# Kernel optimization log

Hardware: AMD Instinct MI355X
Metric: run time of the kernel (lower is better)

## Reference

```python
import jax, jax.numpy as jnp
import numpy as np


def setup_inputs() -> dict:
    key = jax.random.key(0)
    ks = jax.random.split(key, 8)
    B, N, D = 8, 2048, 128
    s = 1.0 / float(np.sqrt(D))
    node = jax.random.normal(ks[0], (B, N, D), dtype=jnp.float32)
    node_mask = jax.random.randint(ks[1], (B, N), 0, 2, dtype=jnp.int32)
    punctuation_graph = jax.random.randint(ks[2], (B, N, N), 0, 2, dtype=jnp.int32)
    w_nw = jax.random.uniform(ks[3], (1, D), jnp.float32, -s, s)
    b_nw = jax.random.uniform(ks[4], (1,), jnp.float32, -s, s)
    w_self = jax.random.uniform(ks[5], (D, D), jnp.float32, -s, s)
    b_self = jax.random.uniform(ks[6], (D,), jnp.float32, -s, s)
    w_punct = jax.random.uniform(ks[7], (D, D), jnp.float32, -s, s)
    return {"node": node, "node_mask": node_mask, "punctuation_graph": punctuation_graph,
            "w_nw": w_nw, "b_nw": b_nw, "w_self": w_self, "b_self": b_self,
            "w_punct": w_punct, "iteration_steps": 2}


def reference(node, node_mask, punctuation_graph, w_nw, b_nw, w_self, b_self, w_punct, iteration_steps):
    B, N, D = node.shape
    # dd_graph = mask outer product with zeroed diagonal; graph = dd_graph * punctuation_graph
    eye = jnp.eye(N, dtype=punctuation_graph.dtype)
    dd = node_mask[:, None, :] * node_mask[:, :, None] * (1 - eye)[None, :, :]  # [B,N,N]
    graph = dd * punctuation_graph  # [B,N,N] int, binary
    nbr_num = graph.sum(-1)  # [B,N]
    # replace_masked_values(nbr_num, nbr_num>=1, 1): nodes with no neighbors get denom 1
    nbr_f = jnp.where(nbr_num >= 1, nbr_num.astype(node.dtype), jnp.asarray(1.0, node.dtype))
    gmask = graph > 0
    weights = []
    x = node
    for _ in range(iteration_steps):  # small fixed step count
        dw = jax.nn.sigmoid(jnp.einsum('bnd,od->bno', x, w_nw) + b_nw)[..., 0]  # [B,N]
        weights.append(dw)
        self_info = jnp.einsum('bnd,ed->bne', x, w_self) + b_self  # [B,N,D]
        info_p = jnp.einsum('bnd,ed->bne', x, w_punct)  # [B,N,D]
        # node_weight[b,i,j] = dw[b,j] where graph[b,i,j] else 0
        nw = jnp.where(gmask, dw[:, None, :], jnp.asarray(0.0, x.dtype))  # [B,N,N]
        agg = jnp.einsum('bnm,bmd->bnd', nw, info_p) / nbr_f[..., None]
        x = jax.nn.relu(self_info + agg)
    all_weight = jnp.stack(weights, axis=1)  # [B, steps, N]
    return x, all_weight
```

## Files before the change

kernel.cpp:

```cpp
#include <hip/hip_runtime.h>
#include <hip/hip_bf16.h>

#define BB 8
#define NN 2048
#define DD 128

typedef __attribute__((ext_vector_type(8))) __bf16 bf16x8;
typedef __attribute__((ext_vector_type(4))) float f32x4;
typedef __attribute__((ext_vector_type(4))) int   i32x4;

static __device__ __forceinline__ unsigned short f2bf(float f) {
    union { float f; unsigned u; } v; v.f = f;
    unsigned r = (v.u + 0x7FFFu + ((v.u >> 16) & 1u)) >> 16;
    return (unsigned short)r;
}
static __device__ __forceinline__ float bf2f(unsigned short b) {
    union { unsigned u; float f; } v; v.u = ((unsigned)b) << 16;
    return v.f;
}

__global__ __launch_bounds__(256) void kernP2(
    const int* __restrict__ punct, const int* __restrict__ mask,
    const float* __restrict__ w_self, const float* __restrict__ w_punct,
    unsigned* __restrict__ pk, float* __restrict__ scale_g, float* __restrict__ pdm_g,
    unsigned short* __restrict__ wsb, unsigned short* __restrict__ wpb)
{
    const int bid = blockIdx.x;
    const int t = threadIdx.x;

    if (bid >= 2048) {
        const int cb = bid - 2048;
        const float* src = (cb < 8) ? w_self : w_punct;
        unsigned short* dst = (cb < 8) ? wsb : wpb;
        const size_t i0 = (size_t)(cb & 7) * 2048 + (size_t)t * 8;
        f32x4 a = *(const f32x4*)(src + i0);
        f32x4 c = *(const f32x4*)(src + i0 + 4);
        unsigned q0 = f2bf(a.x) | ((unsigned)f2bf(a.y) << 16);
        unsigned q1 = f2bf(a.z) | ((unsigned)f2bf(a.w) << 16);
        unsigned q2 = f2bf(c.x) | ((unsigned)f2bf(c.y) << 16);
        unsigned q3 = f2bf(c.z) | ((unsigned)f2bf(c.w) << 16);
        i32x4 pw = {(int)q0, (int)q1, (int)q2, (int)q3};
        *(i32x4*)(dst + i0) = pw;
        return;
    }

    const int wave = t >> 6, lane = t & 63;
    const int row0 = bid * 8 + wave * 2;
    const int b = row0 >> 11;
    const int* mrow = mask + (size_t)b * NN;

    unsigned mreg = 0;
    #pragma unroll
    for (int g = 0; g < 8; ++g) {
        i32x4 m = *(const i32x4*)(mrow + g * 256 + lane * 4);
        unsigned nib = (m.x & 1) | ((m.y & 1) << 1) | ((m.z & 1) << 2) | ((m.w & 1) << 3);
        mreg |= nib << (4 * g);
    }

    #pragma unroll
    for (int r = 0; r < 2; ++r) {
        const int row = row0 + r;
        const int i = row & (NN - 1);
        const int* prow = punct + (size_t)row * NN;
        unsigned* pkrow = pk + (size_t)row * 64;

        int acc = 0;
        #pragma unroll
        for (int g = 0; g < 8; ++g) {
            i32x4 v = *(const i32x4*)(prow + g * 256 + lane * 4);
            unsigned nib = (v.x & 1) | ((v.y & 1) << 1) | ((v.z & 1) << 2) | ((v.w & 1) << 3);
            nib &= (mreg >> (4 * g)) & 0xFu;
            acc += __popc(nib);
            if (((i >> 8) == g) && (((i >> 2) & 63) == lane))
                acc += (int)((nib >> (i & 3)) & 1u) << 16;
            unsigned p1 = __shfl_xor(nib, 1, 64);
            unsigned lo = (lane & 1) ? p1 : nib, hi = (lane & 1) ? nib : p1;
            unsigned by = lo | (hi << 4);
            unsigned p2 = __shfl_xor(by, 2, 64);
            lo = (lane & 2) ? p2 : by; hi = (lane & 2) ? by : p2;
            unsigned hf = lo | (hi << 8);
            unsigned p4 = __shfl_xor(hf, 4, 64);
            lo = (lane & 4) ? p4 : hf; hi = (lane & 4) ? hf : p4;
            unsigned wd = lo | (hi << 16);
            if ((lane & 7) == 0) pkrow[g * 8 + (lane >> 3)] = wd;
        }
        #pragma unroll
        for (int o = 32; o > 0; o >>= 1) acc += __shfl_xor(acc, o, 64);
        if (lane == 0) {
            const int nall = acc & 0xFFFF;
            const int pdm  = acc >> 16;
            const int mi   = mrow[i];
            const int nbr  = nall - pdm;
            scale_g[row] = mi ? 1.f / (float)(nbr < 1 ? 1 : nbr) : 0.f;
            pdm_g[row]   = (float)pdm;
        }
    }
}

template <bool PRECONV>
static __device__ __forceinline__ void kernB_body(
    int n0, const float* __restrict__ x,
    const float* __restrict__ w_nw,  const float* __restrict__ b_nw,
    const void* __restrict__ wself_p, const float* __restrict__ b_self,
    const void* __restrict__ wpunct_p,
    float* __restrict__ si_out,
    unsigned short* __restrict__ yne_out,
    unsigned short* __restrict__ yT_out,
    float* __restrict__ aw_out)
{
    __shared__ unsigned short xt[64*32];
    __shared__ unsigned short wst[128*32];
    __shared__ unsigned short wpt[128*32];
    __shared__ float wnw_l[DD];
    __shared__ float red[256];
    __shared__ float dw_l[64];
    __shared__ unsigned short ytl[128*72];

    const int t  = threadIdx.x;
    const int b  = n0 >> 11;
    const int nb = n0 & (NN - 1);

    if (t < DD) wnw_l[t] = w_nw[t];
    __syncthreads();

    const int wave = t >> 6, lane = t & 63;
    const int wm = wave >> 1, wn = wave & 1;
    const int quad = lane >> 4, l16 = lane & 15;

    const int n_loc = t >> 2, dq = t & 3;
    const int we = t >> 1,   wh = t & 1;

    f32x4 accs[2][4] = {}; f32x4 accp[2][4] = {};
    float dwpart = 0.f;

    #pragma unroll
    for (int kk = 0; kk < 4; ++kk) {
        const int k0 = kk * 32;
        {
            const float* xs = x + (size_t)(n0 + n_loc) * DD + k0 + dq * 8;
            f32x4 a = *(const f32x4*)xs;
            f32x4 c = *(const f32x4*)(xs + 4);
            const float* wv = &wnw_l[k0 + dq * 8];
            dwpart += a.x*wv[0] + a.y*wv[1] + a.z*wv[2] + a.w*wv[3]
                    + c.x*wv[4] + c.y*wv[5] + c.z*wv[6] + c.w*wv[7];
            unsigned q0 = f2bf(a.x) | ((unsigned)f2bf(a.y) << 16);
            unsigned q1 = f2bf(a.z) | ((unsigned)f2bf(a.w) << 16);
            unsigned q2 = f2bf(c.x) | ((unsigned)f2bf(c.y) << 16);
            unsigned q3 = f2bf(c.z) | ((unsigned)f2bf(c.w) << 16);
            i32x4 pw = {(int)q0,(int)q1,(int)q2,(int)q3};
            *(i32x4*)&xt[n_loc*32 + dq*8] = pw;
        }
        if (PRECONV) {
            const unsigned short* s1 = (const unsigned short*)wself_p  + (size_t)we * DD + k0 + wh*16;
            const unsigned short* s2 = (const unsigned short*)wpunct_p + (size_t)we * DD + k0 + wh*16;
            i32x4 a0 = *(const i32x4*)s1;
            i32x4 a1 = *(const i32x4*)(s1 + 8);
            *(i32x4*)&wst[we*32 + wh*16]     = a0;
            *(i32x4*)&wst[we*32 + wh*16 + 8] = a1;
            i32x4 c0 = *(const i32x4*)s2;
            i32x4 c1 = *(const i32x4*)(s2 + 8);
            *(i32x4*)&wpt[we*32 + wh*16]     = c0;
            *(i32x4*)&wpt[we*32 + wh*16 + 8] = c1;
        } else {
            const float* s1 = (const float*)wself_p  + (size_t)we * DD + k0 + wh*16;
            const float* s2 = (const float*)wpunct_p + (size_t)we * DD + k0 + wh*16;
            f32x4 a0 = *(const f32x4*)s1;      f32x4 a1 = *(const f32x4*)(s1+4);
            f32x4 a2 = *(const f32x4*)(s1+8);  f32x4 a3 = *(const f32x4*)(s1+12);
            unsigned q0 = f2bf(a0.x) | ((unsigned)f2bf(a0.y)<<16);
            unsigned q1 = f2bf(a0.z) | ((unsigned)f2bf(a0.w)<<16);
            unsigned q2 = f2bf(a1.x) | ((unsigned)f2bf(a1.y)<<16);
            unsigned q3 = f2bf(a1.z) | ((unsigned)f2bf(a1.w)<<16);
            unsigned q4 = f2bf(a2.x) | ((unsigned)f2bf(a2.y)<<16);
            unsigned q5 = f2bf(a2.z) | ((unsigned)f2bf(a2.w)<<16);
            unsigned q6 = f2bf(a3.x) | ((unsigned)f2bf(a3.y)<<16);
            unsigned q7 = f2bf(a3.z) | ((unsigned)f2bf(a3.w)<<16);
            i32x4 pw0 = {(int)q0,(int)q1,(int)q2,(int)q3};
            i32x4 pw1 = {(int)q4,(int)q5,(int)q6,(int)q7};
            *(i32x4*)&wst[we*32 + wh*16]     = pw0;
            *(i32x4*)&wst[we*32 + wh*16 + 8] = pw1;
            f32x4 c0 = *(const f32x4*)s2;      f32x4 c1 = *(const f32x4*)(s2+4);
            f32x4 c2 = *(const f32x4*)(s2+8);  f32x4 c3 = *(const f32x4*)(s2+12);
            unsigned r0 = f2bf(c0.x) | ((unsigned)f2bf(c0.y)<<16);
            unsigned r1 = f2bf(c0.z) | ((unsigned)f2bf(c0.w)<<16);
            unsigned r2 = f2bf(c1.x) | ((unsigned)f2bf(c1.y)<<16);
            unsigned r3 = f2bf(c1.z) | ((unsigned)f2bf(c1.w)<<16);
            unsigned r4 = f2bf(c2.x) | ((unsigned)f2bf(c2.y)<<16);
            unsigned r5 = f2bf(c2.z) | ((unsigned)f2bf(c2.w)<<16);
            unsigned r6 = f2bf(c3.x) | ((unsigned)f2bf(c3.y)<<16);
            unsigned r7 = f2bf(c3.z) | ((unsigned)f2bf(c3.w)<<16);
            i32x4 pv0 = {(int)r0,(int)r1,(int)r2,(int)r3};
            i32x4 pv1 = {(int)r4,(int)r5,(int)r6,(int)r7};
            *(i32x4*)&wpt[we*32 + wh*16]     = pv0;
            *(i32x4*)&wpt[we*32 + wh*16 + 8] = pv1;
        }
        __syncthreads();
        bf16x8 af[2], bs[4], bp[4];
        #pragma unroll
        for (int mt = 0; mt < 2; ++mt)
            af[mt] = *(const bf16x8*)&xt[(wm*32 + mt*16 + l16)*32 + quad*8];
        #pragma unroll
        for (int nt = 0; nt < 4; ++nt) {
            const int er = wn*64 + nt*16 + l16;
            bs[nt] = *(const bf16x8*)&wst[er*32 + quad*8];
            bp[nt] = *(const bf16x8*)&wpt[er*32 + quad*8];
        }
        #pragma unroll
        for (int mt = 0; mt < 2; ++mt)
            #pragma unroll
            for (int nt = 0; nt < 4; ++nt) {
                accs[mt][nt] = __builtin_amdgcn_mfma_f32_16x16x32_bf16(af[mt], bs[nt], accs[mt][nt], 0, 0, 0);
                accp[mt][nt] = __builtin_amdgcn_mfma_f32_16x16x32_bf16(af[mt], bp[nt], accp[mt][nt], 0, 0, 0);
            }
        __syncthreads();
    }

    red[t] = dwpart;
    __syncthreads();
    if (t < 64) {
        float s = red[4*t] + red[4*t+1] + red[4*t+2] + red[4*t+3] + b_nw[0];
        float dv = 1.f / (1.f + __expf(-s));
        dw_l[t] = dv;
        aw_out[(size_t)b * 2 * NN + nb + t] = dv;
    }
    __syncthreads();

    #pragma unroll
    for (int mt = 0; mt < 2; ++mt) {
        #pragma unroll
        for (int nt = 0; nt < 4; ++nt) {
            const int e = wn*64 + nt*16 + l16;
            const float bsv = b_self[e];
            #pragma unroll
            for (int r = 0; r < 4; ++r) {
                const int nl = wm*32 + mt*16 + quad*4 + r;
                const size_t idx = (size_t)(n0 + nl) * DD + e;
                si_out[idx] = accs[mt][nt][r] + bsv;
                const float yv = dw_l[nl] * accp[mt][nt][r];
                const unsigned short ub = f2bf(yv);
                yne_out[idx] = ub;
                ytl[e*72 + nl] = ub;
            }
        }
    }
    __syncthreads();
    {
        const int e = t >> 1, half = t & 1;
        const i32x4* src = (const i32x4*)&ytl[e*72 + half*32];
        i32x4 v0 = src[0], v1 = src[1], v2 = src[2], v3 = src[3];
        i32x4* dst = (i32x4*)(yT_out + (size_t)(b*DD + e) * NN + nb + half*32);
        dst[0] = v0; dst[1] = v1; dst[2] = v2; dst[3] = v3;
    }
}

__global__ __launch_bounds__(256) void kernB0(
    const float* __restrict__ node,
    const float* __restrict__ w_nw, const float* __restrict__ b_nw,
    const float* __restrict__ w_self, const float* __restrict__ b_self,
    const float* __restrict__ w_punct,
    float* __restrict__ si, unsigned short* __restrict__ yne,
    unsigned short* __restrict__ yT, float* __restrict__ aw)
{
    kernB_body<false>(blockIdx.x * 64, node, w_nw, b_nw, w_self, b_self, w_punct,
                      si, yne, yT, aw);
}

__global__ __launch_bounds__(256) void kernB1(
    const float* __restrict__ x,
    const unsigned short* __restrict__ wsb, const unsigned short* __restrict__ wpb,
    const float* __restrict__ w_nw, const float* __restrict__ b_nw,
    const float* __restrict__ b_self,
    float* __restrict__ si, unsigned short* __restrict__ yne,
    unsigned short* __restrict__ yT, float* __restrict__ aw1)
{
    kernB_body<true>(blockIdx.x * 64, x, w_nw, b_nw, wsb, b_self, wpb,
                     si, yne, yT, aw1);
}

__global__ __launch_bounds__(256) void kernC(
    const unsigned* __restrict__ pk,
    const float* __restrict__ scale_g, const float* __restrict__ pdm_g,
    const unsigned short* __restrict__ yT,
    const float* __restrict__ si,
    const unsigned short* __restrict__ yne,
    float* __restrict__ x_out)
{
    __shared__ unsigned pPk[64 * 68];
    __shared__ float scale_l[64];
    __shared__ float pdm_l[64];

    const int t  = threadIdx.x;
    const int b  = blockIdx.x & 7;
    const int i0 = (blockIdx.x >> 3) * 64;
    const size_t rg0 = (size_t)b * NN + i0;

    #pragma unroll
    for (int r = 0; r < 4; ++r) {
        const int u   = r * 256 + t;
        const int row = u >> 4;
        const int wq  = (u & 15) * 4;
        i32x4 v = *(const i32x4*)(pk + (rg0 + row) * 64 + wq);
        *(i32x4*)&pPk[row * 68 + wq] = v;
    }
    if (t < 64) {
        scale_l[t] = scale_g[rg0 + t];
        pdm_l[t]   = pdm_g[rg0 + t];
    }
    __syncthreads();

    const int wn = t >> 6, lane = t & 63;
    const int quad = lane >> 4, l16 = lane & 15;
    const unsigned short* yTb = yT + (size_t)b * DD * NN;

    f32x4 acc[4][2] = {};

    #pragma unroll 4
    for (int kk = 0; kk < 64; ++kk) {
        bf16x8 bfr[2];
        #pragma unroll
        for (int nt = 0; nt < 2; ++nt) {
            const int e = wn*32 + nt*16 + l16;
            bfr[nt] = *(const bf16x8*)(yTb + (size_t)e * NN + kk*32 + quad*8);
        }
        bf16x8 af[4];
        #pragma unroll
        for (int mt = 0; mt < 4; ++mt) {
            const unsigned w = pPk[(mt*16 + l16) * 68 + kk];
            const unsigned by = (w >> (quad * 8)) & 0xFFu;
            i32x4 ex;
            ex.x = ((by &   1u) ? 0x3F80 : 0) | ((by &   2u) ? 0x3F800000 : 0);
            ex.y = ((by &   4u) ? 0x3F80 : 0) | ((by &   8u) ? 0x3F800000 : 0);
            ex.z = ((by &  16u) ? 0x3F80 : 0) | ((by &  32u) ? 0x3F800000 : 0);
            ex.w = ((by &  64u) ? 0x3F80 : 0) | ((by & 128u) ? 0x3F800000 : 0);
            union { i32x4 i; bf16x8 h; } cv; cv.i = ex;
            af[mt] = cv.h;
        }
        #pragma unroll
        for (int mt = 0; mt < 4; ++mt)
            #pragma unroll
            for (int nt = 0; nt < 2; ++nt)
                acc[mt][nt] = __builtin_amdgcn_mfma_f32_16x16x32_bf16(af[mt], bfr[nt], acc[mt][nt], 0, 0, 0);
    }

    #pragma unroll
    for (int mt = 0; mt < 4; ++mt) {
        #pragma unroll
        for (int nt = 0; nt < 2; ++nt) {
            const int e = wn*32 + nt*16 + l16;
            #pragma unroll
            for (int r = 0; r < 4; ++r) {
                const int row = mt*16 + quad*4 + r;
                const size_t idx = (rg0 + row) * DD + e;
                const float yv = bf2f(yne[idx]);
                float v = si[idx] + scale_l[row] * (acc[mt][nt][r] - pdm_l[row] * yv);
                x_out[idx] = fmaxf(v, 0.f);
            }
        }
    }
}

extern "C" void kernel_launch(void* const* d_in, const int* in_sizes, int n_in,
                              void* d_out, int out_size, void* d_ws, size_t ws_size,
                              hipStream_t stream) {
    const float* node   = (const float*)d_in[0];
    const int*   mask   = (const int*)  d_in[1];
    const int*   punct  = (const int*)  d_in[2];
    const float* w_nw   = (const float*)d_in[3];
    const float* b_nw   = (const float*)d_in[4];
    const float* w_self = (const float*)d_in[5];
    const float* b_self = (const float*)d_in[6];
    const float* w_punct= (const float*)d_in[7];

    float* xout = (float*)d_out;
    float* aw   = xout + (size_t)BB * NN * DD;

    char* w = (char*)d_ws;
    float*          si   = (float*)w;
    unsigned short* yne  = (unsigned short*)(w + (8u  << 20));
    unsigned short* yT   = (unsigned short*)(w + (12u << 20));
    unsigned*       pk   = (unsigned*)(w + (16u << 20));
    float*          scl  = (float*)(w + (20u << 20));
    float*          pdm  = (float*)(w + (20u << 20) + (64u << 10));
    unsigned short* wsb  = (unsigned short*)(w + (21u << 20));
    unsigned short* wpb  = (unsigned short*)(w + (21u << 20) + (32u << 10));

    dim3 blk(256);
    kernP2<<<dim3(2064), blk, 0, stream>>>(punct, mask, w_self, w_punct,
                                           pk, scl, pdm, wsb, wpb);
    kernB0<<<dim3(256), blk, 0, stream>>>(node, w_nw, b_nw, w_self, b_self,
                                          w_punct, si, yne, yT, aw);
    kernC<<<dim3(256), blk, 0, stream>>>(pk, scl, pdm, yT, si, yne, xout);
    kernB1<<<dim3(256), blk, 0, stream>>>(xout, wsb, wpb, w_nw, b_nw, b_self,
                                          si, yne, yT, aw + NN);
    kernC<<<dim3(256), blk, 0, stream>>>(pk, scl, pdm, yT, si, yne, xout);
}
```

Before: 289.0 us.

## Skip masked rows in graph packing and split aggregation over more blocks

```diff
diff --git a/kernel.cpp b/kernel.cpp
--- a/kernel.cpp
+++ b/kernel.cpp
@@ -19,7 +19,7 @@
     return v.f;
 }
 
-__global__ __launch_bounds__(256) void kernP2(
+__global__ __launch_bounds__(256) void kernP3(
     const int* __restrict__ punct, const int* __restrict__ mask,
     const float* __restrict__ w_self, const float* __restrict__ w_punct,
     unsigned* __restrict__ pk, float* __restrict__ scale_g, float* __restrict__ pdm_g,
@@ -49,60 +49,57 @@
     const int b = row0 >> 11;
     const int* mrow = mask + (size_t)b * NN;
 
-    unsigned mreg = 0;
-    #pragma unroll
-    for (int g = 0; g < 8; ++g) {
-        i32x4 m = *(const i32x4*)(mrow + g * 256 + lane * 4);
+    unsigned mw = 0;
+    #pragma unroll
+    for (int q = 0; q < 8; ++q) {
+        i32x4 m = *(const i32x4*)(mrow + lane * 32 + q * 4);
         unsigned nib = (m.x & 1) | ((m.y & 1) << 1) | ((m.z & 1) << 2) | ((m.w & 1) << 3);
-        mreg |= nib << (4 * g);
+        mw |= nib << (4 * q);
     }
 
     #pragma unroll
     for (int r = 0; r < 2; ++r) {
         const int row = row0 + r;
         const int i = row & (NN - 1);
+        const int mi = mrow[i];
+        if (mi == 0) {
+            if (lane == 0) { scale_g[row] = 0.f; pdm_g[row] = 0.f; }
+            continue;
+        }
         const int* prow = punct + (size_t)row * NN;
-        unsigned* pkrow = pk + (size_t)row * 64;
-
-        int acc = 0;
-        #pragma unroll
-        for (int g = 0; g < 8; ++g) {
-            i32x4 v = *(const i32x4*)(prow + g * 256 + lane * 4);
-            unsigned nib = (v.x & 1) | ((v.y & 1) << 1) | ((v.z & 1) << 2) | ((v.w & 1) << 3);
-            nib &= (mreg >> (4 * g)) & 0xFu;
-            acc += __popc(nib);
-            if (((i >> 8) == g) && (((i >> 2) & 63) == lane))
-                acc += (int)((nib >> (i & 3)) & 1u) << 16;
-            unsigned p1 = __shfl_xor(nib, 1, 64);
-            unsigned lo = (lane & 1) ? p1 : nib, hi = (lane & 1) ? nib : p1;
-            unsigned by = lo | (hi << 4);
-            unsigned p2 = __shfl_xor(by, 2, 64);
-            lo = (lane & 2) ? p2 : by; hi = (lane & 2) ? by : p2;
-            unsigned hf = lo | (hi << 8);
-            unsigned p4 = __shfl_xor(hf, 4, 64);
-            lo = (lane & 4) ? p4 : hf; hi = (lane & 4) ? hf : p4;
-            unsigned wd = lo | (hi << 16);
-            if ((lane & 7) == 0) pkrow[g * 8 + (lane >> 3)] = wd;
-        }
+        i32x4 v[8];
+        #pragma unroll
+        for (int q = 0; q < 8; ++q)
+            v[q] = *(const i32x4*)(prow + lane * 32 + q * 4);
+        unsigned wd = 0;
+        #pragma unroll
+        for (int q = 0; q < 8; ++q) {
+            unsigned nib = (v[q].x & 1) | ((v[q].y & 1) << 1)
+                         | ((v[q].z & 1) << 2) | ((v[q].w & 1) << 3);
+            wd |= nib << (4 * q);
+        }
+        wd &= mw;
+        pk[(size_t)row * 64 + lane] = wd;
+
+        int acc = __popc(wd);
+        if ((i >> 5) == lane) acc += (int)((wd >> (i & 31)) & 1u) << 16;
         #pragma unroll
         for (int o = 32; o > 0; o >>= 1) acc += __shfl_xor(acc, o, 64);
         if (lane == 0) {
             const int nall = acc & 0xFFFF;
-            const int pdm  = acc >> 16;
-            const int mi   = mrow[i];
-            const int nbr  = nall - pdm;
-            scale_g[row] = mi ? 1.f / (float)(nbr < 1 ? 1 : nbr) : 0.f;
-            pdm_g[row]   = (float)pdm;
-        }
-    }
-}
-
-template <bool PRECONV>
+            const int pd   = acc >> 16;
+            const int nbr  = nall - pd;
+            scale_g[row] = 1.f / (float)(nbr < 1 ? 1 : nbr);
+            pdm_g[row]   = (float)pd;
+        }
+    }
+}
+
 static __device__ __forceinline__ void kernB_body(
     int n0, const float* __restrict__ x,
     const float* __restrict__ w_nw,  const float* __restrict__ b_nw,
-    const void* __restrict__ wself_p, const float* __restrict__ b_self,
-    const void* __restrict__ wpunct_p,
+    const unsigned short* __restrict__ wsb, const float* __restrict__ b_self,
+    const unsigned short* __restrict__ wpb,
     float* __restrict__ si_out,
     unsigned short* __restrict__ yne_out,
     unsigned short* __restrict__ yT_out,
@@ -150,9 +147,9 @@
             i32x4 pw = {(int)q0,(int)q1,(int)q2,(int)q3};
             *(i32x4*)&xt[n_loc*32 + dq*8] = pw;
         }
-        if (PRECONV) {
-            const unsigned short* s1 = (const unsigned short*)wself_p  + (size_t)we * DD + k0 + wh*16;
-            const unsigned short* s2 = (const unsigned short*)wpunct_p + (size_t)we * DD + k0 + wh*16;
+        {
+            const unsigned short* s1 = wsb + (size_t)we * DD + k0 + wh*16;
+            const unsigned short* s2 = wpb + (size_t)we * DD + k0 + wh*16;
             i32x4 a0 = *(const i32x4*)s1;
             i32x4 a1 = *(const i32x4*)(s1 + 8);
             *(i32x4*)&wst[we*32 + wh*16]     = a0;
@@ -161,37 +158,6 @@
             i32x4 c1 = *(const i32x4*)(s2 + 8);
             *(i32x4*)&wpt[we*32 + wh*16]     = c0;
             *(i32x4*)&wpt[we*32 + wh*16 + 8] = c1;
-        } else {
-            const float* s1 = (const float*)wself_p  + (size_t)we * DD + k0 + wh*16;
-            const float* s2 = (const float*)wpunct_p + (size_t)we * DD + k0 + wh*16;
-            f32x4 a0 = *(const f32x4*)s1;      f32x4 a1 = *(const f32x4*)(s1+4);
-            f32x4 a2 = *(const f32x4*)(s1+8);  f32x4 a3 = *(const f32x4*)(s1+12);
-            unsigned q0 = f2bf(a0.x) | ((unsigned)f2bf(a0.y)<<16);
-            unsigned q1 = f2bf(a0.z) | ((unsigned)f2bf(a0.w)<<16);
-            unsigned q2 = f2bf(a1.x) | ((unsigned)f2bf(a1.y)<<16);
-            unsigned q3 = f2bf(a1.z) | ((unsigned)f2bf(a1.w)<<16);
-            unsigned q4 = f2bf(a2.x) | ((unsigned)f2bf(a2.y)<<16);
-            unsigned q5 = f2bf(a2.z) | ((unsigned)f2bf(a2.w)<<16);
-            unsigned q6 = f2bf(a3.x) | ((unsigned)f2bf(a3.y)<<16);
-            unsigned q7 = f2bf(a3.z) | ((unsigned)f2bf(a3.w)<<16);
-            i32x4 pw0 = {(int)q0,(int)q1,(int)q2,(int)q3};
-            i32x4 pw1 = {(int)q4,(int)q5,(int)q6,(int)q7};
-            *(i32x4*)&wst[we*32 + wh*16]     = pw0;
-            *(i32x4*)&wst[we*32 + wh*16 + 8] = pw1;
-            f32x4 c0 = *(const f32x4*)s2;      f32x4 c1 = *(const f32x4*)(s2+4);
-            f32x4 c2 = *(const f32x4*)(s2+8);  f32x4 c3 = *(const f32x4*)(s2+12);
-            unsigned r0 = f2bf(c0.x) | ((unsigned)f2bf(c0.y)<<16);
-            unsigned r1 = f2bf(c0.z) | ((unsigned)f2bf(c0.w)<<16);
-            unsigned r2 = f2bf(c1.x) | ((unsigned)f2bf(c1.y)<<16);
-            unsigned r3 = f2bf(c1.z) | ((unsigned)f2bf(c1.w)<<16);
-            unsigned r4 = f2bf(c2.x) | ((unsigned)f2bf(c2.y)<<16);
-            unsigned r5 = f2bf(c2.z) | ((unsigned)f2bf(c2.w)<<16);
-            unsigned r6 = f2bf(c3.x) | ((unsigned)f2bf(c3.y)<<16);
-            unsigned r7 = f2bf(c3.z) | ((unsigned)f2bf(c3.w)<<16);
-            i32x4 pv0 = {(int)r0,(int)r1,(int)r2,(int)r3};
-            i32x4 pv1 = {(int)r4,(int)r5,(int)r6,(int)r7};
-            *(i32x4*)&wpt[we*32 + wh*16]     = pv0;
-            *(i32x4*)&wpt[we*32 + wh*16 + 8] = pv1;
         }
         __syncthreads();
         bf16x8 af[2], bs[4], bp[4];
@@ -252,31 +218,19 @@
     }
 }
 
-__global__ __launch_bounds__(256) void kernB0(
-    const float* __restrict__ node,
-    const float* __restrict__ w_nw, const float* __restrict__ b_nw,
-    const float* __restrict__ w_self, const float* __restrict__ b_self,
-    const float* __restrict__ w_punct,
-    float* __restrict__ si, unsigned short* __restrict__ yne,
-    unsigned short* __restrict__ yT, float* __restrict__ aw)
-{
-    kernB_body<false>(blockIdx.x * 64, node, w_nw, b_nw, w_self, b_self, w_punct,
-                      si, yne, yT, aw);
-}
-
-__global__ __launch_bounds__(256) void kernB1(
+__global__ __launch_bounds__(256) void kernB(
     const float* __restrict__ x,
     const unsigned short* __restrict__ wsb, const unsigned short* __restrict__ wpb,
     const float* __restrict__ w_nw, const float* __restrict__ b_nw,
     const float* __restrict__ b_self,
     float* __restrict__ si, unsigned short* __restrict__ yne,
-    unsigned short* __restrict__ yT, float* __restrict__ aw1)
+    unsigned short* __restrict__ yT, float* __restrict__ aw_s)
 {
-    kernB_body<true>(blockIdx.x * 64, x, w_nw, b_nw, wsb, b_self, wpb,
-                     si, yne, yT, aw1);
-}
-
-__global__ __launch_bounds__(256) void kernC(
+    kernB_body(blockIdx.x * 64, x, w_nw, b_nw, wsb, b_self, wpb,
+               si, yne, yT, aw_s);
+}
+
+__global__ __launch_bounds__(128) void kernC3(
     const unsigned* __restrict__ pk,
     const float* __restrict__ scale_g, const float* __restrict__ pdm_g,
     const unsigned short* __restrict__ yT,
@@ -284,24 +238,26 @@
     const unsigned short* __restrict__ yne,
     float* __restrict__ x_out)
 {
-    __shared__ unsigned pPk[64 * 68];
-    __shared__ float scale_l[64];
-    __shared__ float pdm_l[64];
-
-    const int t  = threadIdx.x;
-    const int b  = blockIdx.x & 7;
-    const int i0 = (blockIdx.x >> 3) * 64;
+    __shared__ unsigned pPk[32 * 68];
+    __shared__ float scale_l[32];
+    __shared__ float pdm_l[32];
+
+    const int t   = threadIdx.x;
+    const int b   = blockIdx.x & 7;
+    const int idx = blockIdx.x >> 3;
+    const int i0  = (idx >> 1) * 32;
+    const int e0  = (idx & 1) * 64;
     const size_t rg0 = (size_t)b * NN + i0;
 
     #pragma unroll
     for (int r = 0; r < 4; ++r) {
-        const int u   = r * 256 + t;
+        const int u   = r * 128 + t;
         const int row = u >> 4;
         const int wq  = (u & 15) * 4;
         i32x4 v = *(const i32x4*)(pk + (rg0 + row) * 64 + wq);
         *(i32x4*)&pPk[row * 68 + wq] = v;
     }
-    if (t < 64) {
+    if (t < 32) {
         scale_l[t] = scale_g[rg0 + t];
         pdm_l[t]   = pdm_g[rg0 + t];
     }
@@ -311,19 +267,19 @@
     const int quad = lane >> 4, l16 = lane & 15;
     const unsigned short* yTb = yT + (size_t)b * DD * NN;
 
-    f32x4 acc[4][2] = {};
+    f32x4 acc[2][2] = {};
 
     #pragma unroll 4
     for (int kk = 0; kk < 64; ++kk) {
         bf16x8 bfr[2];
         #pragma unroll
         for (int nt = 0; nt < 2; ++nt) {
-            const int e = wn*32 + nt*16 + l16;
+            const int e = e0 + wn*32 + nt*16 + l16;
             bfr[nt] = *(const bf16x8*)(yTb + (size_t)e * NN + kk*32 + quad*8);
         }
-        bf16x8 af[4];
-        #pragma unroll
-        for (int mt = 0; mt < 4; ++mt) {
+        bf16x8 af[2];
+        #pragma unroll
+        for (int mt = 0; mt < 2; ++mt) {
             const unsigned w = pPk[(mt*16 + l16) * 68 + kk];
             const unsigned by = (w >> (quad * 8)) & 0xFFu;
             i32x4 ex;
@@ -335,24 +291,24 @@
             af[mt] = cv.h;
         }
         #pragma unroll
-        for (int mt = 0; mt < 4; ++mt)
+        for (int mt = 0; mt < 2; ++mt)
             #pragma unroll
             for (int nt = 0; nt < 2; ++nt)
                 acc[mt][nt] = __builtin_amdgcn_mfma_f32_16x16x32_bf16(af[mt], bfr[nt], acc[mt][nt], 0, 0, 0);
     }
 
     #pragma unroll
-    for (int mt = 0; mt < 4; ++mt) {
+    for (int mt = 0; mt < 2; ++mt) {
         #pragma unroll
         for (int nt = 0; nt < 2; ++nt) {
-            const int e = wn*32 + nt*16 + l16;
+            const int e = e0 + wn*32 + nt*16 + l16;
             #pragma unroll
             for (int r = 0; r < 4; ++r) {
                 const int row = mt*16 + quad*4 + r;
-                const size_t idx = (rg0 + row) * DD + e;
-                const float yv = bf2f(yne[idx]);
-                float v = si[idx] + scale_l[row] * (acc[mt][nt][r] - pdm_l[row] * yv);
-                x_out[idx] = fmaxf(v, 0.f);
+                const size_t idx2 = (rg0 + row) * DD + e;
+                const float yv = bf2f(yne[idx2]);
+                float v = si[idx2] + scale_l[row] * (acc[mt][nt][r] - pdm_l[row] * yv);
+                x_out[idx2] = fmaxf(v, 0.f);
             }
         }
     }
@@ -383,13 +339,12 @@
     unsigned short* wsb  = (unsigned short*)(w + (21u << 20));
     unsigned short* wpb  = (unsigned short*)(w + (21u << 20) + (32u << 10));
 
-    dim3 blk(256);
-    kernP2<<<dim3(2064), blk, 0, stream>>>(punct, mask, w_self, w_punct,
-                                           pk, scl, pdm, wsb, wpb);
-    kernB0<<<dim3(256), blk, 0, stream>>>(node, w_nw, b_nw, w_self, b_self,
-                                          w_punct, si, yne, yT, aw);
-    kernC<<<dim3(256), blk, 0, stream>>>(pk, scl, pdm, yT, si, yne, xout);
-    kernB1<<<dim3(256), blk, 0, stream>>>(xout, wsb, wpb, w_nw, b_nw, b_self,
-                                          si, yne, yT, aw + NN);
-    kernC<<<dim3(256), blk, 0, stream>>>(pk, scl, pdm, yT, si, yne, xout);
-}
+    kernP3<<<dim3(2064), dim3(256), 0, stream>>>(punct, mask, w_self, w_punct,
+                                                 pk, scl, pdm, wsb, wpb);
+    kernB <<<dim3(256),  dim3(256), 0, stream>>>(node, wsb, wpb, w_nw, b_nw,
+                                                 b_self, si, yne, yT, aw);
+    kernC3<<<dim3(1024), dim3(128), 0, stream>>>(pk, scl, pdm, yT, si, yne, xout);
+    kernB <<<dim3(256),  dim3(256), 0, stream>>>(xout, wsb, wpb, w_nw, b_nw,
+                                                 b_self, si, yne, yT, aw + NN);
+    kernC3<<<dim3(1024), dim3(128), 0, stream>>>(pk, scl, pdm, yT, si, yne, xout);
+}
```

New measurement: 294.9 us. 1.02x slower.
